# Kernel tuning notes

Measured on AMD Instinct MI355X. Metric: run time of the kernel, lower is better.

The kernel has to match this reference:

```python
import jax, jax.numpy as jnp
import numpy as np

B, S, D, NH = 2, 2048, 2048, 16
HD = D // NH  # 128


def setup_inputs() -> dict:
    key = jax.random.key(0)
    ks = jax.random.split(key, 7)
    s = 1.0 / np.sqrt(D)
    return {
        "hidden_states": jax.random.normal(ks[0], (B, S, D), dtype=jnp.float32),
        "Wq": jax.random.normal(ks[1], (D, D), dtype=jnp.float32) * s,
        "Wk": jax.random.normal(ks[2], (D, D), dtype=jnp.float32) * s,
        "Wv": jax.random.normal(ks[3], (D, D), dtype=jnp.float32) * s,
        "Wo": jax.random.normal(ks[4], (D, D), dtype=jnp.float32) * s,
        # phase projections: hidden -> num_heads (zero-init in the module; use small
        # random values so the phase path is numerically exercised)
        "Wpq": jax.random.normal(ks[5], (D, NH), dtype=jnp.float32) * 0.02,
        "Wpk": jax.random.normal(ks[6], (D, NH), dtype=jnp.float32) * 0.02,
    }


def reference(hidden_states, Wq, Wk, Wv, Wo, Wpq, Wpk):
    x = hidden_states  # [B,S,D]
    # ---- base_attn: standard causal multi-head self-attention ----
    q = (x @ Wq).reshape(B, S, NH, HD).transpose(0, 2, 1, 3)  # [B,H,S,hd]
    k = (x @ Wk).reshape(B, S, NH, HD).transpose(0, 2, 1, 3)
    v = (x @ Wv).reshape(B, S, NH, HD).transpose(0, 2, 1, 3)
    scores = jnp.einsum("bhqd,bhkd->bhqk", q, k) / np.sqrt(HD)  # [B,H,S,S]
    causal = jnp.tril(jnp.ones((S, S), dtype=bool))
    scores = jnp.where(causal, scores, jnp.float32(-1e9))
    probs = jax.nn.softmax(scores, axis=-1)
    ctx = jnp.einsum("bhqk,bhkd->bhqd", probs, v)  # [B,H,S,hd]
    attn_output = ctx.transpose(0, 2, 1, 3).reshape(B, S, D) @ Wo  # [B,S,D]
    # ---- phase modulation ----
    # original: cos(pq[b,q,None,h] - pk[b,None,k,h]).mean(dims=(k,h))  -> [B,S]
    # identity: cos(a-b) = cos a * cos b + sin a * sin b lets us avoid the
    # [B,S,S,H] tensor; the math is identical.
    pq = x @ Wpq  # [B,S,H]
    pk = x @ Wpk  # [B,S,H]
    Ck = jnp.cos(pk).sum(axis=1)  # [B,H]
    Sk = jnp.sin(pk).sum(axis=1)  # [B,H]
    phase_mod = (jnp.cos(pq) * Ck[:, None, :] + jnp.sin(pq) * Sk[:, None, :]).sum(-1) / (S * NH)  # [B,S]
    return attn_output * (1.0 + 0.1 * phase_mod[..., None])
```

## Files before the change

### kernel.cpp

```cpp
#include <hip/hip_runtime.h>
#include <hip/hip_bf16.h>

typedef __attribute__((ext_vector_type(8))) short short8;
typedef __attribute__((ext_vector_type(4))) float f32x4;
typedef __attribute__((ext_vector_type(16))) float f32x16;
typedef __attribute__((ext_vector_type(4))) int i32x4;
typedef unsigned short u16;

#define S_LEN 2048
#define D_DIM 2048
#define NHEAD 16
#define HDIM 128
#define M_ROWS 4096

#define MFMA(a,b,c) __builtin_amdgcn_mfma_f32_16x16x32_bf16(a,b,c,0,0,0)
#define MFMA32(a,b,c) __builtin_amdgcn_mfma_f32_32x32x16_bf16(a,b,c,0,0,0)

__device__ __forceinline__ u16 f2bf(float f) {
  union { float f; unsigned u; } v; v.f = f;
  unsigned r = v.u + 0x7fffu + ((v.u >> 16) & 1u);
  return (u16)(r >> 16);
}

__device__ __forceinline__ void async16(void* lds, const void* g) {
  __builtin_amdgcn_global_load_lds(
      (const __attribute__((address_space(1))) unsigned*)g,
      (__attribute__((address_space(3))) unsigned*)lds, 16, 0, 0);
}

__device__ __forceinline__ unsigned cvtpk(float lo, float hi) {
  unsigned r;
  asm("v_cvt_pk_bf16_f32 %0, %1, %2" : "=v"(r) : "v"(lo), "v"(hi));
  return r;
}
__device__ __forceinline__ void plswap(unsigned& x, unsigned& y) {
  asm("v_permlane32_swap_b32 %0, %1" : "+v"(x), "+v"(y));
}

__global__ void k_cvt_x(const float* __restrict__ x, u16* __restrict__ xb) {
  int i = blockIdx.x * 256 + threadIdx.x;
  float4 v = reinterpret_cast<const float4*>(x)[i];
  ushort4 o;
  o.x = f2bf(v.x); o.y = f2bf(v.y); o.z = f2bf(v.z); o.w = f2bf(v.w);
  reinterpret_cast<ushort4*>(xb)[i] = o;
}

__global__ void k_cvt_wt(const float* __restrict__ W, u16* __restrict__ Wt) {
  __shared__ u16 tile[32][33];
  int n0 = blockIdx.x * 32, k0 = blockIdx.y * 32;
  int tx = threadIdx.x & 31, ty = threadIdx.x >> 5;
#pragma unroll
  for (int i = 0; i < 4; i++)
    tile[ty + i * 8][tx] = f2bf(W[(size_t)(k0 + ty + i * 8) * D_DIM + n0 + tx]);
  __syncthreads();
#pragma unroll
  for (int i = 0; i < 4; i++)
    Wt[(size_t)(n0 + ty + i * 8) * D_DIM + k0 + tx] = tile[tx][ty + i * 8];
}

__global__ void k_vtrans(const u16* __restrict__ V, u16* __restrict__ Vt) {
  __shared__ u16 tile[32][33];
  int s0 = blockIdx.x * 32, d0 = blockIdx.y * 32, bh = blockIdx.z;
  const u16* Vp = V + (size_t)bh * S_LEN * HDIM;
  u16* Vtp = Vt + (size_t)bh * HDIM * S_LEN;
  int tx = threadIdx.x & 31, ty = threadIdx.x >> 5;
#pragma unroll
  for (int i = 0; i < 4; i++)
    tile[ty + i * 8][tx] = Vp[(size_t)(s0 + ty + i * 8) * HDIM + d0 + tx];
  __syncthreads();
#pragma unroll
  for (int i = 0; i < 4; i++)
    Vtp[(size_t)(d0 + ty + i * 8) * S_LEN + s0 + tx] = tile[tx][ty + i * 8];
}

template <int MODE>
__global__ __launch_bounds__(256) void k_gemm(const u16* __restrict__ A,
                                              const u16* __restrict__ Bt,
                                              void* __restrict__ outp,
                                              const float* __restrict__ fac) {
  __shared__ u16 As[128 * 32];
  __shared__ u16 Bs[128 * 32];
  const int m0 = blockIdx.y * 128, n0 = blockIdx.x * 128;
  const int t = threadIdx.x;
  const int w = t >> 6, l = t & 63;
  const int wr = (w >> 1) * 64, wc = (w & 1) * 64;
  const int lr = l & 15, lk = (l >> 4) * 8;
  f32x4 acc[4][4] = {};

  for (int k0 = 0; k0 < D_DIM; k0 += 32) {
#pragma unroll
    for (int i = 0; i < 2; i++) {
      const int ib = i * 256 + w * 64;
      const int idx = ib + l;
      const int row = idx >> 2, kq = idx & 3;
      async16(As + ib * 8, A + (size_t)(m0 + row) * D_DIM + k0 + kq * 8);
      async16(Bs + ib * 8, Bt + (size_t)(n0 + row) * D_DIM + k0 + kq * 8);
    }
    __syncthreads();
    short8 af[4], bfr[4];
#pragma unroll
    for (int mi = 0; mi < 4; mi++)
      af[mi] = *reinterpret_cast<const short8*>(As + (wr + mi * 16 + lr) * 32 + lk);
#pragma unroll
    for (int ni = 0; ni < 4; ni++)
      bfr[ni] = *reinterpret_cast<const short8*>(Bs + (wc + ni * 16 + lr) * 32 + lk);
#pragma unroll
    for (int mi = 0; mi < 4; mi++)
#pragma unroll
      for (int ni = 0; ni < 4; ni++)
        acc[mi][ni] = MFMA(af[mi], bfr[ni], acc[mi][ni]);
    __syncthreads();
  }

#pragma unroll
  for (int mi = 0; mi < 4; mi++) {
#pragma unroll
    for (int ni = 0; ni < 4; ni++) {
#pragma unroll
      for (int r = 0; r < 4; r++) {
        const int row = m0 + wr + mi * 16 + (l >> 4) * 4 + r;
        const int col = n0 + wc + ni * 16 + lr;
        float v = acc[mi][ni][r];
        if (MODE == 0) {
          ((u16*)outp)[(((size_t)((row >> 11) * NHEAD + (col >> 7))) * S_LEN +
                        (row & 2047)) * HDIM + (col & 127)] = f2bf(v);
        } else {
          ((float*)outp)[(size_t)row * D_DIM + col] = v * (1.0f + 0.1f * fac[row]);
        }
      }
    }
  }
}

__global__ __launch_bounds__(64) void k_phase_proj(const float* __restrict__ x,
                                                   const float* __restrict__ Wpq,
                                                   const float* __restrict__ Wpk,
                                                   float* __restrict__ pq,
                                                   float* __restrict__ pk) {
  int m = blockIdx.x;
  int l = threadIdx.x;
  int h = l & 15, part = l >> 4;
  const float* xr = x + (size_t)m * D_DIM + part * 512;
  float sq = 0.f, sk = 0.f;
  for (int k = 0; k < 512; k++) {
    float xv = xr[k];
    int kk = part * 512 + k;
    sq += xv * Wpq[(size_t)kk * NHEAD + h];
    sk += xv * Wpk[(size_t)kk * NHEAD + h];
  }
  sq += __shfl_xor(sq, 16); sq += __shfl_xor(sq, 32);
  sk += __shfl_xor(sk, 16); sk += __shfl_xor(sk, 32);
  if (l < 16) {
    pq[(size_t)m * NHEAD + l] = sq;
    pk[(size_t)m * NHEAD + l] = sk;
  }
}

__device__ __forceinline__ float wave_sum(float v) {
  v += __shfl_xor(v, 1);  v += __shfl_xor(v, 2);  v += __shfl_xor(v, 4);
  v += __shfl_xor(v, 8);  v += __shfl_xor(v, 16); v += __shfl_xor(v, 32);
  return v;
}

__global__ void k_phase_ck(const float* __restrict__ pk, float* __restrict__ Ck,
                           float* __restrict__ Sk) {
  int bh = blockIdx.x, b = bh >> 4, h = bh & 15;
  float c = 0.f, s = 0.f;
  for (int ss = threadIdx.x; ss < S_LEN; ss += 256) {
    float v = pk[((size_t)b * S_LEN + ss) * NHEAD + h];
    c += cosf(v); s += sinf(v);
  }
  c = wave_sum(c); s = wave_sum(s);
  __shared__ float rc[4], rs[4];
  int wv = threadIdx.x >> 6;
  if ((threadIdx.x & 63) == 0) { rc[wv] = c; rs[wv] = s; }
  __syncthreads();
  if (threadIdx.x == 0) {
    Ck[bh] = rc[0] + rc[1] + rc[2] + rc[3];
    Sk[bh] = rs[0] + rs[1] + rs[2] + rs[3];
  }
}

__global__ void k_phase_mod(const float* __restrict__ pq, const float* __restrict__ Ck,
                            const float* __restrict__ Sk, float* __restrict__ pm) {
  int m = blockIdx.x * 256 + threadIdx.x;
  int b = m >> 11;
  float a = 0.f;
#pragma unroll
  for (int h = 0; h < NHEAD; h++) {
    float v = pq[(size_t)m * NHEAD + h];
    a += cosf(v) * Ck[b * NHEAD + h] + sinf(v) * Sk[b * NHEAD + h];
  }
  pm[m] = a * (1.0f / (S_LEN * NHEAD));
}

__global__ __launch_bounds__(256, 2) void k_attn(const u16* __restrict__ Q,
                                                 const u16* __restrict__ K,
                                                 const u16* __restrict__ Vt,
                                                 u16* __restrict__ ctx) {
  const int bh = blockIdx.x;
  const int gy = blockIdx.y;
  const int g = (gy < 8) ? (15 - gy) : (gy - 8);
  const int b = bh >> 4, h = bh & 15;
  const int t = threadIdx.x;
  const int w = t >> 6, l = t & 63;
  const int ln = l & 31, hi = l >> 5;
  const int q0w = g * 128 + w * 32;
  const int qq = q0w + ln;
  const float scale = 0.08838834764831845f;

  const u16* Qp = Q + (size_t)bh * S_LEN * HDIM;
  const char* Kg = (const char*)(K + (size_t)bh * S_LEN * HDIM);
  const char* Vg = (const char*)(Vt + (size_t)bh * HDIM * S_LEN);

  __shared__ __align__(16) char Ks[16384];
  __shared__ __align__(16) char Vs[16384];

  short8 qf[8];
#pragma unroll
  for (int c = 0; c < 8; c++)
    qf[c] = *reinterpret_cast<const short8*>(Qp + (size_t)qq * HDIM + c * 16 + hi * 8);

  f32x16 o[4];
#pragma unroll
  for (int ds = 0; ds < 4; ds++)
#pragma unroll
    for (int r = 0; r < 16; r++) o[ds][r] = 0.f;
  float mrun = -1e30f, lsum = 0.f;

  const int kend = (g + 1) * 128;
  for (int k0 = 0; k0 < kend; k0 += 64) {
#pragma unroll
    for (int i = 0; i < 4; i++) {
      const int key = i * 16 + w * 4 + (l >> 4);
      async16(Ks + i * 4096 + w * 1024,
              Kg + (size_t)(k0 + key) * 256 + (((l & 15) * 16) ^ ((key & 7) << 4)));
      const int d = i * 32 + w * 8 + (l >> 3);
      async16(Vs + i * 4096 + w * 1024,
              Vg + (size_t)d * (S_LEN * 2) + k0 * 2 + (((l & 7) * 16) ^ ((d & 7) << 4)));
    }
    __syncthreads();
    if (k0 < q0w + 32) {
      f32x16 s[2];
#pragma unroll
      for (int ks = 0; ks < 2; ks++)
#pragma unroll
        for (int r = 0; r < 16; r++) s[ks][r] = 0.f;
      __builtin_amdgcn_s_setprio(1);
#pragma unroll
      for (int ks = 0; ks < 2; ks++) {
        const int key = ks * 32 + ln;
        const char* kb = Ks + key * 256;
        const unsigned swzk = (unsigned)((key & 7) << 4);
#pragma unroll
        for (int c = 0; c < 8; c++) {
          const short8 kf = *reinterpret_cast<const short8*>(
              kb + (((unsigned)(c * 32 + hi * 16)) ^ swzk));
          s[ks] = MFMA32(kf, qf[c], s[ks]);
        }
      }
      __builtin_amdgcn_s_setprio(0);
      float p[32];
      float mx = -1e30f;
#pragma unroll
      for (int ks = 0; ks < 2; ks++)
#pragma unroll
        for (int r = 0; r < 16; r++) {
          const int key = k0 + ks * 32 + (r & 3) + 8 * (r >> 2) + 4 * hi;
          const float v = (key <= qq) ? s[ks][r] * scale : -1e30f;
          p[ks * 16 + r] = v;
          mx = fmaxf(mx, v);
        }
      mx = fmaxf(mx, __shfl_xor(mx, 32));
      const float nm = fmaxf(mrun, mx);
      const float f = __expf(mrun - nm);
      float rs = 0.f;
#pragma unroll
      for (int i = 0; i < 32; i++) { p[i] = __expf(p[i] - nm); rs += p[i]; }
      rs += __shfl_xor(rs, 32);
      lsum = lsum * f + rs;
      mrun = nm;
#pragma unroll
      for (int ds = 0; ds < 4; ds++)
#pragma unroll
        for (int r = 0; r < 16; r++) o[ds][r] *= f;
      short8 bfr[4];
#pragma unroll
      for (int sub = 0; sub < 2; sub++) {
#pragma unroll
        for (int half = 0; half < 2; half++) {
          const int pb = sub * 16 + half * 8;
          unsigned X1 = cvtpk(p[pb + 0], p[pb + 1]);
          unsigned X2 = cvtpk(p[pb + 2], p[pb + 3]);
          unsigned Y1 = cvtpk(p[pb + 4], p[pb + 5]);
          unsigned Y2 = cvtpk(p[pb + 6], p[pb + 7]);
          plswap(X1, Y1);
          plswap(X2, Y2);
          i32x4 bw;
          bw[0] = (int)X1; bw[1] = (int)X2; bw[2] = (int)Y1; bw[3] = (int)Y2;
          bfr[sub * 2 + half] = __builtin_bit_cast(short8, bw);
        }
      }
      __builtin_amdgcn_s_setprio(1);
#pragma unroll
      for (int ds = 0; ds < 4; ds++) {
        const int d = ds * 32 + ln;
        const char* vb = Vs + d * 128;
        const unsigned swzv = (unsigned)((d & 7) << 4);
#pragma unroll
        for (int slot = 0; slot < 4; slot++) {
          const short8 vf = *reinterpret_cast<const short8*>(
              vb + (((unsigned)(slot * 32 + hi * 16)) ^ swzv));
          o[ds] = MFMA32(vf, bfr[slot], o[ds]);
        }
      }
      __builtin_amdgcn_s_setprio(0);
    }
    __syncthreads();
  }

  const float rl = 1.0f / lsum;
#pragma unroll
  for (int ds = 0; ds < 4; ds++) {
#pragma unroll
    for (int rq = 0; rq < 4; rq++) {
      const int d = ds * 32 + 8 * rq + 4 * hi;
      ushort4 pk4;
      pk4.x = f2bf(o[ds][rq * 4 + 0] * rl);
      pk4.y = f2bf(o[ds][rq * 4 + 1] * rl);
      pk4.z = f2bf(o[ds][rq * 4 + 2] * rl);
      pk4.w = f2bf(o[ds][rq * 4 + 3] * rl);
      *reinterpret_cast<ushort4*>(ctx + ((size_t)(b * S_LEN + qq)) * D_DIM + h * HDIM + d) = pk4;
    }
  }
}

extern "C" void kernel_launch(void* const* d_in, const int* in_sizes, int n_in,
                              void* d_out, int out_size, void* d_ws, size_t ws_size,
                              hipStream_t stream) {
  const float* x   = (const float*)d_in[0];
  const float* Wq  = (const float*)d_in[1];
  const float* Wk  = (const float*)d_in[2];
  const float* Wv  = (const float*)d_in[3];
  const float* Wo  = (const float*)d_in[4];
  const float* Wpq = (const float*)d_in[5];
  const float* Wpk = (const float*)d_in[6];

  char* ws = (char*)d_ws;
  u16* xb   = (u16*)(ws + 0);
  u16* Wqt  = (u16*)(ws + 16777216);
  u16* Wkt  = (u16*)(ws + 25165824);
  u16* Wvt  = (u16*)(ws + 33554432);
  u16* Wot  = (u16*)(ws + 41943040);
  u16* Qb   = (u16*)(ws + 50331648);
  u16* Kb   = (u16*)(ws + 67108864);
  u16* Vb   = (u16*)(ws + 83886080);
  u16* Vt   = (u16*)(ws + 100663296);
  float* pq = (float*)(ws + 117440512);
  float* pk = (float*)(ws + 117702656);
  float* Ck = (float*)(ws + 117964800);
  float* Sk = (float*)(ws + 117964928);
  float* pm = (float*)(ws + 117965056);

  k_cvt_x<<<dim3(M_ROWS * D_DIM / 1024), 256, 0, stream>>>(x, xb);
  k_cvt_wt<<<dim3(64, 64), 256, 0, stream>>>(Wq, Wqt);
  k_cvt_wt<<<dim3(64, 64), 256, 0, stream>>>(Wk, Wkt);
  k_cvt_wt<<<dim3(64, 64), 256, 0, stream>>>(Wv, Wvt);
  k_cvt_wt<<<dim3(64, 64), 256, 0, stream>>>(Wo, Wot);

  k_gemm<0><<<dim3(16, 32), 256, 0, stream>>>(xb, Wqt, Qb, nullptr);
  k_gemm<0><<<dim3(16, 32), 256, 0, stream>>>(xb, Wkt, Kb, nullptr);
  k_gemm<0><<<dim3(16, 32), 256, 0, stream>>>(xb, Wvt, Vb, nullptr);

  k_vtrans<<<dim3(64, 4, 32), 256, 0, stream>>>(Vb, Vt);

  k_phase_proj<<<dim3(M_ROWS), 64, 0, stream>>>(x, Wpq, Wpk, pq, pk);
  k_phase_ck<<<dim3(32), 256, 0, stream>>>(pk, Ck, Sk);
  k_phase_mod<<<dim3(16), 256, 0, stream>>>(pq, Ck, Sk, pm);

  k_attn<<<dim3(32, 16), 256, 0, stream>>>(Qb, Kb, Vt, Vb );

  k_gemm<1><<<dim3(16, 32), 256, 0, stream>>>(Vb , Wot, (void*)d_out, pm);
}
```

Baseline: 367.2 us.

## Replace GEMM with 256x256 double-buffered swizzled MFMA kernel fusing QKV projections

Swaps the 128x128 single-buffered GEMM for a 512-thread, 256x256-tile kernel with K=64 steps, double-buffered LDS and XOR-swizzled addressing to avoid bank conflicts. Loads for the next tile are interleaved with four MFMA phases using barriers and s_setprio. The three Q/K/V projections become one launch over a 6144-wide N dimension, which assumes Wqt/Wkt/Wvt and Qb/Kb/Vb sit contiguously in the workspace. This cuts launch count and global traffic per FLOP, at the cost of 128KB LDS per block, heavier register use and fewer blocks for the output GEMM.

```diff
diff --git a/kernel.cpp b/kernel.cpp
--- a/kernel.cpp
+++ b/kernel.cpp
@@ -74,56 +74,121 @@
 }
 
 template <int MODE>
-__global__ __launch_bounds__(256) void k_gemm(const u16* __restrict__ A,
-                                              const u16* __restrict__ Bt,
-                                              void* __restrict__ outp,
-                                              const float* __restrict__ fac) {
-  __shared__ u16 As[128 * 32];
-  __shared__ u16 Bs[128 * 32];
-  const int m0 = blockIdx.y * 128, n0 = blockIdx.x * 128;
+__global__ __launch_bounds__(512, 2) void k_gemm8(const u16* __restrict__ A,
+                                                  const u16* __restrict__ Bt,
+                                                  void* __restrict__ outp,
+                                                  const float* __restrict__ fac) {
+  __shared__ __align__(16) char lds[131072];
+  const int m0 = blockIdx.y * 256, n0 = blockIdx.x * 256;
   const int t = threadIdx.x;
   const int w = t >> 6, l = t & 63;
-  const int wr = (w >> 1) * 64, wc = (w & 1) * 64;
-  const int lr = l & 15, lk = (l >> 4) * 8;
-  f32x4 acc[4][4] = {};
-
-  for (int k0 = 0; k0 < D_DIM; k0 += 32) {
-#pragma unroll
-    for (int i = 0; i < 2; i++) {
-      const int ib = i * 256 + w * 64;
-      const int idx = ib + l;
-      const int row = idx >> 2, kq = idx & 3;
-      async16(As + ib * 8, A + (size_t)(m0 + row) * D_DIM + k0 + kq * 8);
-      async16(Bs + ib * 8, Bt + (size_t)(n0 + row) * D_DIM + k0 + kq * 8);
-    }
-    __syncthreads();
-    short8 af[4], bfr[4];
-#pragma unroll
-    for (int mi = 0; mi < 4; mi++)
-      af[mi] = *reinterpret_cast<const short8*>(As + (wr + mi * 16 + lr) * 32 + lk);
-#pragma unroll
-    for (int ni = 0; ni < 4; ni++)
-      bfr[ni] = *reinterpret_cast<const short8*>(Bs + (wc + ni * 16 + lr) * 32 + lk);
-#pragma unroll
-    for (int mi = 0; mi < 4; mi++)
-#pragma unroll
-      for (int ni = 0; ni < 4; ni++)
-        acc[mi][ni] = MFMA(af[mi], bfr[ni], acc[mi][ni]);
-    __syncthreads();
-  }
-
-#pragma unroll
-  for (int mi = 0; mi < 4; mi++) {
+  const int wr = (w >> 2) * 128, wc = (w & 3) * 64;
+  const int lr = l & 15, lq = l >> 4;
+  const char* Ab = (const char*)A;
+  const char* Bb = (const char*)Bt;
+
+  f32x4 acc[8][4] = {};
+
+#define STAGE_HALF(MATB, R0, ISB, H, TT, BUF)                                     \
+  {                                                                               \
+    _Pragma("unroll") for (int j = 0; j < 2; j++) {                               \
+      const int p = (j * 8 + w) * 1024 + l * 16;                                  \
+      const int lg = p ^ (((p >> 7) & 7) << 4);                                   \
+      async16(lds + (BUF) * 65536 + (ISB) * 32768 + (H) * 16384 + (j * 8 + w) * 1024, \
+              (MATB) + (size_t)((R0) + (H) * 128 + (lg >> 7)) * 4096 + (TT) * 128 \
+                  + (lg & 127));                                                  \
+    }                                                                             \
+  }
+
+  STAGE_HALF(Ab, m0, 0, 0, 0, 0);
+  STAGE_HALF(Bb, n0, 1, 0, 0, 0);
+  STAGE_HALF(Ab, m0, 0, 1, 0, 0);
+  STAGE_HALF(Bb, n0, 1, 1, 0, 0);
+  asm volatile("s_waitcnt vmcnt(2)" ::: "memory");
+  __builtin_amdgcn_s_barrier();
+
+  const int NT = D_DIM / 64;
+  for (int tt = 0; tt < NT; tt++) {
+    const int buf = tt & 1, nbuf = buf ^ 1;
+    const bool pf = (tt + 1 < NT);
+    const char* Ar = lds + buf * 65536;
+    const char* Br = lds + buf * 65536 + 32768;
+    short8 a0[4][2], a1[4][2], b0[2][2], b1[2][2];
+
+    auto rdA = [&](short8 af[4][2], int mh) {
+#pragma unroll
+      for (int mi = 0; mi < 4; mi++)
+#pragma unroll
+        for (int ks = 0; ks < 2; ks++) {
+          const int row = wr + mh * 64 + mi * 16 + lr;
+          af[mi][ks] = *reinterpret_cast<const short8*>(
+              Ar + ((row * 128 + ks * 64 + lq * 16) ^ ((row & 7) << 4)));
+        }
+    };
+    auto rdB = [&](short8 bf[2][2], int nh) {
+#pragma unroll
+      for (int ni = 0; ni < 2; ni++)
+#pragma unroll
+        for (int ks = 0; ks < 2; ks++) {
+          const int row = wc + nh * 32 + ni * 16 + lr;
+          bf[ni][ks] = *reinterpret_cast<const short8*>(
+              Br + ((row * 128 + ks * 64 + lq * 16) ^ ((row & 7) << 4)));
+        }
+    };
+
+#define PHASE_MFMA(MH, NH, AF, BF)                                    \
+  {                                                                   \
+    asm volatile("" ::: "memory");                                    \
+    __builtin_amdgcn_s_barrier();                                     \
+    __builtin_amdgcn_s_setprio(1);                                    \
+    _Pragma("unroll") for (int mi = 0; mi < 4; mi++)                  \
+    _Pragma("unroll") for (int ni = 0; ni < 2; ni++)                  \
+    _Pragma("unroll") for (int ks = 0; ks < 2; ks++)                  \
+      acc[(MH) * 4 + mi][(NH) * 2 + ni] =                             \
+          MFMA(AF[mi][ks], BF[ni][ks], acc[(MH) * 4 + mi][(NH) * 2 + ni]); \
+    __builtin_amdgcn_s_setprio(0);                                    \
+    asm volatile("" ::: "memory");                                    \
+    __builtin_amdgcn_s_barrier();                                     \
+  }
+
+    asm volatile("s_waitcnt vmcnt(2)" ::: "memory");
+    rdA(a0, 0); rdB(b0, 0);
+    if (pf) STAGE_HALF(Ab, m0, 0, 0, tt + 1, nbuf);
+    PHASE_MFMA(0, 0, a0, b0);
+
+    if (pf) { asm volatile("s_waitcnt vmcnt(2)" ::: "memory"); }
+    else    { asm volatile("s_waitcnt vmcnt(0)" ::: "memory"); }
+    rdA(a1, 1);
+    if (pf) STAGE_HALF(Bb, n0, 1, 0, tt + 1, nbuf);
+    PHASE_MFMA(1, 0, a1, b0);
+
+    rdB(b1, 1);
+    if (pf) STAGE_HALF(Ab, m0, 0, 1, tt + 1, nbuf);
+    PHASE_MFMA(1, 1, a1, b1);
+
+    asm volatile("s_waitcnt vmcnt(2)" ::: "memory");
+    rdA(a0, 0);
+    if (pf) STAGE_HALF(Bb, n0, 1, 1, tt + 1, nbuf);
+    PHASE_MFMA(0, 1, a0, b1);
+  }
+#undef STAGE_HALF
+#undef PHASE_MFMA
+
+#pragma unroll
+  for (int mi = 0; mi < 8; mi++) {
 #pragma unroll
     for (int ni = 0; ni < 4; ni++) {
 #pragma unroll
       for (int r = 0; r < 4; r++) {
-        const int row = m0 + wr + mi * 16 + (l >> 4) * 4 + r;
+        const int row = m0 + wr + mi * 16 + lq * 4 + r;
         const int col = n0 + wc + ni * 16 + lr;
-        float v = acc[mi][ni][r];
+        const float v = acc[mi][ni][r];
         if (MODE == 0) {
-          ((u16*)outp)[(((size_t)((row >> 11) * NHEAD + (col >> 7))) * S_LEN +
-                        (row & 2047)) * HDIM + (col & 127)] = f2bf(v);
+          const int mat = col >> 11;
+          const int hh = (col >> 7) & 15;
+          ((u16*)outp)[(size_t)mat * 8388608 +
+                       (((size_t)((row >> 11) * NHEAD + hh)) * S_LEN + (row & 2047)) * HDIM +
+                       (col & 127)] = f2bf(v);
         } else {
           ((float*)outp)[(size_t)row * D_DIM + col] = v * (1.0f + 0.1f * fac[row]);
         }
@@ -368,9 +433,7 @@
   k_cvt_wt<<<dim3(64, 64), 256, 0, stream>>>(Wv, Wvt);
   k_cvt_wt<<<dim3(64, 64), 256, 0, stream>>>(Wo, Wot);
 
-  k_gemm<0><<<dim3(16, 32), 256, 0, stream>>>(xb, Wqt, Qb, nullptr);
-  k_gemm<0><<<dim3(16, 32), 256, 0, stream>>>(xb, Wkt, Kb, nullptr);
-  k_gemm<0><<<dim3(16, 32), 256, 0, stream>>>(xb, Wvt, Vb, nullptr);
+  k_gemm8<0><<<dim3(24, 16), 512, 0, stream>>>(xb, Wqt, Qb, nullptr);
 
   k_vtrans<<<dim3(64, 4, 32), 256, 0, stream>>>(Vb, Vt);
 
@@ -380,5 +443,5 @@
 
   k_attn<<<dim3(32, 16), 256, 0, stream>>>(Qb, Kb, Vt, Vb );
 
-  k_gemm<1><<<dim3(16, 32), 256, 0, stream>>>(Vb , Wot, (void*)d_out, pm);
-}
+  k_gemm8<1><<<dim3(8, 16), 512, 0, stream>>>(Vb , Wot, (void*)d_out, pm);
+}
```

New measurement: 350.9 us. -4.5%, faster.

## Fuse QKV projections into one double-buffered 256-row GEMM with swizzled LDS

Applied to the files above, without the earlier changes.

Replaces the simple 128x128 single-buffered GEMM with a 512-thread, 256-row tile kernel that double-buffers 64-wide K slices through swizzled LDS, using explicit vmcnt waits and barriers so global loads overlap MFMA work. The three Q/K/V projections become one launch over a concatenated weight (relies on Wqt/Wkt/Wvt being contiguous in the workspace) and write into consecutive Q/K/V buffers. The output projection uses the same kernel with a narrower N tile. It also widens the K swizzle in attention to 16 rows. The larger tiles raise register and LDS pressure, and the fused launch depends on the workspace layout.

```diff
diff --git a/kernel.cpp b/kernel.cpp
--- a/kernel.cpp
+++ b/kernel.cpp
@@ -73,57 +73,106 @@
     Vtp[(size_t)(d0 + ty + i * 8) * S_LEN + s0 + tx] = tile[tx][ty + i * 8];
 }
 
-template <int MODE>
-__global__ __launch_bounds__(256) void k_gemm(const u16* __restrict__ A,
-                                              const u16* __restrict__ Bt,
-                                              void* __restrict__ outp,
-                                              const float* __restrict__ fac) {
-  __shared__ u16 As[128 * 32];
-  __shared__ u16 Bs[128 * 32];
-  const int m0 = blockIdx.y * 128, n0 = blockIdx.x * 128;
+template <int NFRAG, int MODE>
+__global__ __launch_bounds__(512, 2) void k_gemm2p(const u16* __restrict__ A,
+                                                   const u16* __restrict__ Bt,
+                                                   void* __restrict__ outp,
+                                                   const float* __restrict__ fac) {
+  constexpr int BN = NFRAG * 64;
+  constexpr int ASUB = 16384;
+  constexpr int BSUB = BN * 64;
+  constexpr int BBASE = 4 * ASUB;
+  constexpr int LPU = 2 + NFRAG / 2;
+  __shared__ __align__(16) char lds[4 * ASUB + 4 * BSUB];
+  const int m0 = blockIdx.y * 256, n0 = blockIdx.x * BN;
   const int t = threadIdx.x;
   const int w = t >> 6, l = t & 63;
-  const int wr = (w >> 1) * 64, wc = (w & 1) * 64;
-  const int lr = l & 15, lk = (l >> 4) * 8;
-  f32x4 acc[4][4] = {};
-
-  for (int k0 = 0; k0 < D_DIM; k0 += 32) {
-#pragma unroll
-    for (int i = 0; i < 2; i++) {
-      const int ib = i * 256 + w * 64;
-      const int idx = ib + l;
-      const int row = idx >> 2, kq = idx & 3;
-      async16(As + ib * 8, A + (size_t)(m0 + row) * D_DIM + k0 + kq * 8);
-      async16(Bs + ib * 8, Bt + (size_t)(n0 + row) * D_DIM + k0 + kq * 8);
-    }
-    __syncthreads();
-    short8 af[4], bfr[4];
-#pragma unroll
-    for (int mi = 0; mi < 4; mi++)
-      af[mi] = *reinterpret_cast<const short8*>(As + (wr + mi * 16 + lr) * 32 + lk);
-#pragma unroll
-    for (int ni = 0; ni < 4; ni++)
-      bfr[ni] = *reinterpret_cast<const short8*>(Bs + (wc + ni * 16 + lr) * 32 + lk);
-#pragma unroll
-    for (int mi = 0; mi < 4; mi++)
-#pragma unroll
-      for (int ni = 0; ni < 4; ni++)
-        acc[mi][ni] = MFMA(af[mi], bfr[ni], acc[mi][ni]);
-    __syncthreads();
-  }
-
-#pragma unroll
-  for (int mi = 0; mi < 4; mi++) {
-#pragma unroll
-    for (int ni = 0; ni < 4; ni++) {
+  const int wr = (w >> 2) * 128, wc = (w & 3) * (BN / 4);
+  const int lr = l & 15, lq = l >> 4;
+  const char* Ab = (const char*)A;
+  const char* Bb = (const char*)Bt;
+
+  f32x4 acc[8][NFRAG] = {};
+
+  auto stage_unit = [&](int tt, int s, int buf) {
+#pragma unroll
+    for (int j = 0; j < 2; j++) {
+      const int p = j * 8192 + w * 1024 + l * 16;
+      const int row = p >> 6, slot = (p >> 4) & 3;
+      async16(lds + buf * 2 * ASUB + s * ASUB + j * 8192 + w * 1024,
+              Ab + (size_t)(m0 + row) * 4096 + tt * 128 + s * 64 +
+                  ((slot ^ ((row >> 1) & 3)) * 16));
+    }
+#pragma unroll
+    for (int j = 0; j < NFRAG / 2; j++) {
+      const int p = j * 8192 + w * 1024 + l * 16;
+      const int row = p >> 6, slot = (p >> 4) & 3;
+      async16(lds + BBASE + buf * 2 * BSUB + s * BSUB + j * 8192 + w * 1024,
+              Bb + (size_t)(n0 + row) * 4096 + tt * 128 + s * 64 +
+                  ((slot ^ ((row >> 1) & 3)) * 16));
+    }
+  };
+
+  auto phase = [&](int buf, int s) {
+    const char* Ar = lds + buf * 2 * ASUB + s * ASUB;
+    const char* Br = lds + BBASE + buf * 2 * BSUB + s * BSUB;
+    short8 af[8], bf[NFRAG];
+#pragma unroll
+    for (int mi = 0; mi < 8; mi++) {
+      const int row = wr + mi * 16 + lr;
+      af[mi] = *reinterpret_cast<const short8*>(
+          Ar + row * 64 + ((lq ^ ((row >> 1) & 3)) * 16));
+    }
+#pragma unroll
+    for (int ni = 0; ni < NFRAG; ni++) {
+      const int row = wc + ni * 16 + lr;
+      bf[ni] = *reinterpret_cast<const short8*>(
+          Br + row * 64 + ((lq ^ ((row >> 1) & 3)) * 16));
+    }
+    __builtin_amdgcn_s_setprio(1);
+#pragma unroll
+    for (int mi = 0; mi < 8; mi++)
+#pragma unroll
+      for (int ni = 0; ni < NFRAG; ni++)
+        acc[mi][ni] = MFMA(af[mi], bf[ni], acc[mi][ni]);
+    __builtin_amdgcn_s_setprio(0);
+  };
+
+  stage_unit(0, 0, 0);
+  stage_unit(0, 1, 0);
+
+  const int NT = D_DIM / 64;
+  for (int tt = 0; tt < NT; tt++) {
+    const int buf = tt & 1;
+    const bool pf = (tt + 1 < NT);
+    asm volatile("s_waitcnt vmcnt(%0)" :: "n"(LPU) : "memory");
+    __builtin_amdgcn_s_barrier();
+    asm volatile("" ::: "memory");
+    if (pf) stage_unit(tt + 1, 0, buf ^ 1);
+    phase(buf, 0);
+    if (pf) asm volatile("s_waitcnt vmcnt(%0)" :: "n"(LPU) : "memory");
+    else    asm volatile("s_waitcnt vmcnt(0)" ::: "memory");
+    __builtin_amdgcn_s_barrier();
+    asm volatile("" ::: "memory");
+    if (pf) stage_unit(tt + 1, 1, buf ^ 1);
+    phase(buf, 1);
+  }
+
+#pragma unroll
+  for (int mi = 0; mi < 8; mi++) {
+#pragma unroll
+    for (int ni = 0; ni < NFRAG; ni++) {
 #pragma unroll
       for (int r = 0; r < 4; r++) {
-        const int row = m0 + wr + mi * 16 + (l >> 4) * 4 + r;
+        const int row = m0 + wr + mi * 16 + lq * 4 + r;
         const int col = n0 + wc + ni * 16 + lr;
-        float v = acc[mi][ni][r];
+        const float v = acc[mi][ni][r];
         if (MODE == 0) {
-          ((u16*)outp)[(((size_t)((row >> 11) * NHEAD + (col >> 7))) * S_LEN +
-                        (row & 2047)) * HDIM + (col & 127)] = f2bf(v);
+          const int mat = col >> 11;
+          const int hh = (col >> 7) & 15;
+          ((u16*)outp)[(size_t)mat * 8388608 +
+                       (((size_t)((row >> 11) * NHEAD + hh)) * S_LEN + (row & 2047)) * HDIM +
+                       (col & 127)] = f2bf(v);
         } else {
           ((float*)outp)[(size_t)row * D_DIM + col] = v * (1.0f + 0.1f * fac[row]);
         }
@@ -234,7 +283,7 @@
     for (int i = 0; i < 4; i++) {
       const int key = i * 16 + w * 4 + (l >> 4);
       async16(Ks + i * 4096 + w * 1024,
-              Kg + (size_t)(k0 + key) * 256 + (((l & 15) * 16) ^ ((key & 7) << 4)));
+              Kg + (size_t)(k0 + key) * 256 + (((l & 15) * 16) ^ ((key & 15) << 4)));
       const int d = i * 32 + w * 8 + (l >> 3);
       async16(Vs + i * 4096 + w * 1024,
               Vg + (size_t)d * (S_LEN * 2) + k0 * 2 + (((l & 7) * 16) ^ ((d & 7) << 4)));
@@ -251,7 +300,7 @@
       for (int ks = 0; ks < 2; ks++) {
         const int key = ks * 32 + ln;
         const char* kb = Ks + key * 256;
-        const unsigned swzk = (unsigned)((key & 7) << 4);
+        const unsigned swzk = (unsigned)((key & 15) << 4);
 #pragma unroll
         for (int c = 0; c < 8; c++) {
           const short8 kf = *reinterpret_cast<const short8*>(
@@ -368,9 +417,7 @@
   k_cvt_wt<<<dim3(64, 64), 256, 0, stream>>>(Wv, Wvt);
   k_cvt_wt<<<dim3(64, 64), 256, 0, stream>>>(Wo, Wot);
 
-  k_gemm<0><<<dim3(16, 32), 256, 0, stream>>>(xb, Wqt, Qb, nullptr);
-  k_gemm<0><<<dim3(16, 32), 256, 0, stream>>>(xb, Wkt, Kb, nullptr);
-  k_gemm<0><<<dim3(16, 32), 256, 0, stream>>>(xb, Wvt, Vb, nullptr);
+  k_gemm2p<4, 0><<<dim3(24, 16), 512, 0, stream>>>(xb, Wqt, Qb, nullptr);
 
   k_vtrans<<<dim3(64, 4, 32), 256, 0, stream>>>(Vb, Vt);
 
@@ -380,5 +427,5 @@
 
   k_attn<<<dim3(32, 16), 256, 0, stream>>>(Qb, Kb, Vt, Vb );
 
-  k_gemm<1><<<dim3(16, 32), 256, 0, stream>>>(Vb , Wot, (void*)d_out, pm);
-}
+  k_gemm2p<2, 1><<<dim3(16, 16), 512, 0, stream>>>(Vb , Wot, (void*)d_out, pm);
+}
```

Measured after the change: 327.4 us. 10.8% less time.
